# Kernel tuning notes

Measured on AMD Instinct MI355X. Metric: run time of the kernel, lower is better.

Reference implementation:

```python
import jax, jax.numpy as jnp
import numpy as np

N_ELEM = 10   # len(EnvPara.ELEMENTS)
N_ATOMS = 100000
N_DIM = 256


def setup_inputs() -> dict:
    key = jax.random.key(0)
    k = jax.random.split(key, 5)
    return {
        "input_tensor": jax.random.normal(k[0], (N_ATOMS, N_DIM), jnp.float32),
        "species": jax.random.randint(k[1], (N_ATOMS,), 0, N_ELEM, dtype=jnp.int64),
        "W1": jax.random.normal(k[2], (N_ELEM, N_DIM, N_DIM), jnp.float32) / np.sqrt(N_DIM).astype(np.float32),
        "b1": jnp.zeros((N_ELEM, N_DIM), jnp.float32),
        "W2": jax.random.normal(k[3], (N_ELEM, N_DIM, 1), jnp.float32) / np.sqrt(N_DIM).astype(np.float32),
        "b2": jnp.zeros((N_ELEM, 1), jnp.float32),
    }


def _element_linear(x, species, W, b):
    # Species-routed linear: each atom uses the weight/bias of its element.
    # Loop over the small fixed element set (N_ELEM=10) to avoid materializing
    # a [n_atoms, d_in, d_out] gathered-weight tensor.
    out = jnp.zeros((x.shape[0], W.shape[2]), dtype=x.dtype)
    for e in range(W.shape[0]):
        mask = (species == e)[:, None]                      # [n_atoms, 1]
        out = out + jnp.where(mask, x @ W[e] + b[e], jnp.zeros((), x.dtype))
    return out


def reference(input_tensor, species, W1, b1, W2, b2):
    # layer2(silu(layer1(x)))
    h = _element_linear(input_tensor, species, W1, b1)      # [n_atoms, n_dim]
    h = jax.nn.silu(h)                                      # way=0 -> plain SiLU
    return _element_linear(h, species, W2, b2)              # [n_atoms, 1]
```

## Files before the change

### kernel.cpp

```cpp
#include <hip/hip_runtime.h>
#include <hip/hip_bf16.h>
#include <stdint.h>


#define NDIM 256
#define CHUNKS 16
#define BCHUNK 16384
#define TROWS 32
#define ROWB 1040

typedef __attribute__((ext_vector_type(8))) short short8;
typedef __attribute__((ext_vector_type(8))) unsigned short ushort8;
typedef __attribute__((ext_vector_type(4))) float f32x4;

__device__ __forceinline__ unsigned short f2bf(float f) {
  unsigned u = __float_as_uint(f);
  u = (u + 0x7FFFu + ((u >> 16) & 1u)) >> 16;
  return (unsigned short)u;
}

__device__ __forceinline__ void gload_lds16(const void* gsrc, void* ldst) {
  __builtin_amdgcn_global_load_lds(
      (const __attribute__((address_space(1))) unsigned*)gsrc,
      (__attribute__((address_space(3))) unsigned*)(uintptr_t)(unsigned)(uintptr_t)ldst,
      16, 0, 0);
}

__device__ __forceinline__ short8 cvt8(float4 lo, float4 hi) {
  union { short8 s; unsigned u[4]; } r;
  __hip_bfloat162 t;
  t = __float22bfloat162_rn(make_float2(lo.x, lo.y)); r.u[0] = *(unsigned*)&t;
  t = __float22bfloat162_rn(make_float2(lo.z, lo.w)); r.u[1] = *(unsigned*)&t;
  t = __float22bfloat162_rn(make_float2(hi.x, hi.y)); r.u[2] = *(unsigned*)&t;
  t = __float22bfloat162_rn(make_float2(hi.z, hi.w)); r.u[3] = *(unsigned*)&t;
  return r.s;
}


__global__ void convw_k(const float* __restrict__ W1, unsigned short* __restrict__ wt, int NE) {
  int t = blockIdx.x * 256 + threadIdx.x;
  if (t >= NE * 8192) return;
  int n = t & 255;
  int g = (t >> 8) & 3;
  int step = (t >> 10) & 7;
  int e = t >> 13;
  int k0 = step * 32 + g * 8;
  const float* src = W1 + ((size_t)e << 16) + (size_t)k0 * NDIM + n;
  unsigned short v[8];
  #pragma unroll
  for (int j = 0; j < 8; ++j) v[j] = f2bf(src[j * NDIM]);
  char* chunk = (char*)wt + (size_t)(e * 8 + step) * BCHUNK;
  unsigned off = ((unsigned)(n * 64 + g * 16)) ^ ((unsigned)((n & 7) << 4));
  *(ushort8*)(chunk + off) = *(ushort8*)v;
}

__global__ void bhist_k(const int* __restrict__ sp, int n, int* __restrict__ bc, int NE) {
  __shared__ int wc[4][16];
  int tid = threadIdx.x;
  int i = blockIdx.x * 256 + tid;
  int s = (i < n) ? sp[i] : -1;
  int w = tid >> 6, lane = tid & 63;
  for (int e = 0; e < NE; ++e) {
    unsigned long long m = __ballot(s == e);
    if (lane == 0) wc[w][e] = __popcll(m);
  }
  __syncthreads();
  if (tid < NE) bc[blockIdx.x * NE + tid] = wc[0][tid] + wc[1][tid] + wc[2][tid] + wc[3][tid];
}

__global__ void scan_k(const int* __restrict__ bc, int* __restrict__ bo,
                       int* __restrict__ atom_start, int* __restrict__ tile_off,
                       int nblocks, int NE) {
  __shared__ int csum[256];
  __shared__ int coff[256];
  __shared__ int stot[16];
  __shared__ int sbase[16];
  int tid = threadIdx.x;
  int per = (nblocks + CHUNKS - 1) / CHUNKS;
  int e = tid / CHUNKS, c = tid % CHUNKS;
  int b0 = c * per, b1 = b0 + per; if (b1 > nblocks) b1 = nblocks;
  if (tid < NE * CHUNKS) {
    int s = 0;
    for (int b = b0; b < b1; ++b) s += bc[b * NE + e];
    csum[tid] = s;
  }
  __syncthreads();
  if (tid < NE) {
    int r = 0;
    for (int c2 = 0; c2 < CHUNKS; ++c2) { coff[tid * CHUNKS + c2] = r; r += csum[tid * CHUNKS + c2]; }
    stot[tid] = r;
  }
  __syncthreads();
  if (tid == 0) {
    int a = 0, t = 0;
    for (int e2 = 0; e2 < NE; ++e2) {
      sbase[e2] = a;
      atom_start[e2] = a; tile_off[e2] = t;
      a += stot[e2]; t += (stot[e2] + TROWS - 1) / TROWS;
    }
    atom_start[NE] = a; tile_off[NE] = t;
  }
  __syncthreads();
  if (tid < NE * CHUNKS) {
    int run = sbase[e] + coff[tid];
    for (int b = b0; b < b1; ++b) { bo[b * NE + e] = run; run += bc[b * NE + e]; }
  }
}

__global__ void dscatter_k(const int* __restrict__ sp, int n, const int* __restrict__ bo,
                           int* __restrict__ sorted, int NE) {
  __shared__ int wc[4][16];
  int tid = threadIdx.x;
  int i = blockIdx.x * 256 + tid;
  int s = (i < n) ? sp[i] : -1;
  int w = tid >> 6, lane = tid & 63;
  for (int e = 0; e < NE; ++e) {
    unsigned long long m = __ballot(s == e);
    if (lane == 0) wc[w][e] = __popcll(m);
  }
  __syncthreads();
  for (int e = 0; e < NE; ++e) {
    unsigned long long m = __ballot(s == e);
    if (s == e) {
      int wpre = 0;
      for (int w2 = 0; w2 < 4; ++w2) if (w2 < w) wpre += wc[w2][e];
      int rank = __popcll(m & ((1ull << lane) - 1ull));
      sorted[bo[blockIdx.x * NE + e] + wpre + rank] = i;
    }
  }
}


__global__ __launch_bounds__(512, 4) void gemm_k(
    const float* __restrict__ x, const unsigned short* __restrict__ wt,
    const float* __restrict__ b1, const float* __restrict__ w2,
    const float* __restrict__ b2, const int* __restrict__ sorted,
    const int* __restrict__ atom_start, const int* __restrict__ tile_off,
    float* __restrict__ out, int NE)
{
  __shared__ __align__(16) char smem[TROWS * ROWB + 1024];
  char* ldsA = smem;
  float* partLds = (float*)(smem + TROWS * ROWB);

  int b = blockIdx.x;
  if (b >= tile_off[NE]) return;
  int e = NE - 1;
  for (int i = 0; i < NE; ++i) { if (b < tile_off[i + 1]) { e = i; break; } }
  int t = b - tile_off[e];
  int rowStart = atom_start[e] + t * TROWS;
  int rowsValid = atom_start[e + 1] - rowStart;
  if (rowsValid > TROWS) rowsValid = TROWS;

  int tid = threadIdx.x;
  int lane = tid & 63, wid = tid >> 6;
  int lr = lane & 15, lg = lane >> 4;

  #pragma unroll
  for (int i = 0; i < 4; ++i) {
    int r = wid * 4 + i;
    int rr = (r < rowsValid) ? r : (rowsValid - 1);
    int atom = sorted[rowStart + rr];
    gload_lds16(x + (size_t)atom * NDIM + lane * 4, ldsA + r * ROWB);
  }

  const char* wbase = (const char*)wt + (size_t)e * 8 * BCHUNK;
  short8 bf[2][8];
  #pragma unroll
  for (int nf = 0; nf < 2; ++nf) {
    int n = wid * 32 + nf * 16 + lr;
    unsigned off = ((unsigned)(n * 64 + lg * 16)) ^ ((unsigned)((n & 7) << 4));
    #pragma unroll
    for (int s = 0; s < 8; ++s)
      bf[nf][s] = *(const short8*)(wbase + (size_t)s * BCHUNK + off);
  }

  f32x4 acc[2][2];
  const f32x4 zero = {0.f, 0.f, 0.f, 0.f};
  #pragma unroll
  for (int i = 0; i < 2; ++i)
    #pragma unroll
    for (int j = 0; j < 2; ++j) acc[i][j] = zero;

  __syncthreads();

  #pragma unroll
  for (int step = 0; step < 8; ++step) {
    int k0 = step * 32;
    short8 af[2];
    #pragma unroll
    for (int mf = 0; mf < 2; ++mf) {
      int r = mf * 16 + lr;
      const char* p = ldsA + r * ROWB + (k0 + lg * 8) * 4;
      float4 lo = *(const float4*)p;
      float4 hi = *(const float4*)(p + 16);
      af[mf] = cvt8(lo, hi);
    }
    #pragma unroll
    for (int mf = 0; mf < 2; ++mf)
      #pragma unroll
      for (int nf = 0; nf < 2; ++nf)
        acc[mf][nf] = __builtin_amdgcn_mfma_f32_16x16x32_bf16(af[mf], bf[nf][step], acc[mf][nf], 0, 0, 0);
  }

  const float* b1p = b1 + (size_t)e * NDIM;
  const float* w2p = w2 + (size_t)e * NDIM;
  float psum[2][4];
  #pragma unroll
  for (int mf = 0; mf < 2; ++mf)
    #pragma unroll
    for (int rg = 0; rg < 4; ++rg) psum[mf][rg] = 0.f;

  #pragma unroll
  for (int nf = 0; nf < 2; ++nf) {
    int ncol = wid * 32 + nf * 16 + lr;
    float bb = b1p[ncol];
    float wv = w2p[ncol];
    #pragma unroll
    for (int mf = 0; mf < 2; ++mf)
      #pragma unroll
      for (int rg = 0; rg < 4; ++rg) {
        float h = acc[mf][nf][rg] + bb;
        float sv = h * __builtin_amdgcn_rcpf(1.f + __expf(-h));
        psum[mf][rg] += sv * wv;
      }
  }

  #pragma unroll
  for (int mf = 0; mf < 2; ++mf)
    #pragma unroll
    for (int rg = 0; rg < 4; ++rg) {
      float v = psum[mf][rg];
      v += __shfl_xor(v, 1, 64);
      v += __shfl_xor(v, 2, 64);
      v += __shfl_xor(v, 4, 64);
      v += __shfl_xor(v, 8, 64);
      psum[mf][rg] = v;
    }

  if (lr == 0) {
    #pragma unroll
    for (int mf = 0; mf < 2; ++mf)
      #pragma unroll
      for (int rg = 0; rg < 4; ++rg)
        partLds[wid * TROWS + mf * 16 + lg * 4 + rg] = psum[mf][rg];
  }
  __syncthreads();
  if (tid < TROWS && tid < rowsValid) {
    float s = b2[e];
    #pragma unroll
    for (int w = 0; w < 8; ++w) s += partLds[w * TROWS + tid];
    out[sorted[rowStart + tid]] = s;
  }
}


extern "C" void kernel_launch(void* const* d_in, const int* in_sizes, int n_in,
                              void* d_out, int out_size, void* d_ws, size_t ws_size,
                              hipStream_t stream) {
  const float* x  = (const float*)d_in[0];
  const int*   sp = (const int*)d_in[1];
  const float* W1 = (const float*)d_in[2];
  const float* b1 = (const float*)d_in[3];
  const float* W2 = (const float*)d_in[4];
  const float* b2 = (const float*)d_in[5];
  float* out = (float*)d_out;

  int n_atoms = in_sizes[0] / NDIM;
  int NE = in_sizes[2] / (NDIM * NDIM);
  int nblocks = (n_atoms + 255) / 256;

  char* wsb = (char*)d_ws;
  size_t o = 0;
  int* bc = (int*)(wsb + o);         o += ((size_t)nblocks * NE * 4 + 255) & ~(size_t)255;
  int* bo = (int*)(wsb + o);         o += ((size_t)nblocks * NE * 4 + 255) & ~(size_t)255;
  int* atom_start = (int*)(wsb + o); o += 256;
  int* tile_off   = (int*)(wsb + o); o += 256;
  int* sorted     = (int*)(wsb + o); o += ((size_t)n_atoms * 4 + 255) & ~(size_t)255;
  unsigned short* wt = (unsigned short*)(wsb + o);

  hipLaunchKernelGGL(convw_k, dim3((NE * 8192 + 255) / 256), dim3(256), 0, stream,
                     W1, wt, NE);
  hipLaunchKernelGGL(bhist_k, dim3(nblocks), dim3(256), 0, stream, sp, n_atoms, bc, NE);
  hipLaunchKernelGGL(scan_k, dim3(1), dim3(256), 0, stream, bc, bo, atom_start, tile_off,
                     nblocks, NE);
  hipLaunchKernelGGL(dscatter_k, dim3(nblocks), dim3(256), 0, stream, sp, n_atoms, bo,
                     sorted, NE);

  int maxTiles = (n_atoms + TROWS - 1) / TROWS + NE;
  hipLaunchKernelGGL(gemm_k, dim3(maxTiles), dim3(512), 0, stream,
                     x, wt, b1, W2, b2, sorted, atom_start, tile_off, out, NE);
}
```

Before: 70.70 us.

## Make gemm kernel persistent with double-buffered row staging and weight reuse

The expert GEMM kernel becomes a persistent grid of 512 blocks, each walking a contiguous range of 32-row tiles. Per-element bf16 weight fragments, bias and W2 values stay in registers until the element changes, instead of being reloaded for every tile. The next tile's gathered input rows are prefetched into a second LDS buffer while the current tile is computed. The costs are doubled LDS per block, which may limit blocks per CU, and the risk of load imbalance from the static contiguous tile split.

New measurement: 69.83 us. Within noise of the previous version (-1.2%).

```diff
diff --git a/kernel.cpp b/kernel.cpp
--- a/kernel.cpp
+++ b/kernel.cpp
@@ -138,118 +138,140 @@
     const int* __restrict__ atom_start, const int* __restrict__ tile_off,
     float* __restrict__ out, int NE)
 {
-  __shared__ __align__(16) char smem[TROWS * ROWB + 1024];
-  char* ldsA = smem;
-  float* partLds = (float*)(smem + TROWS * ROWB);
-
-  int b = blockIdx.x;
-  if (b >= tile_off[NE]) return;
-  int e = NE - 1;
-  for (int i = 0; i < NE; ++i) { if (b < tile_off[i + 1]) { e = i; break; } }
-  int t = b - tile_off[e];
-  int rowStart = atom_start[e] + t * TROWS;
-  int rowsValid = atom_start[e + 1] - rowStart;
-  if (rowsValid > TROWS) rowsValid = TROWS;
-
-  int tid = threadIdx.x;
-  int lane = tid & 63, wid = tid >> 6;
+  __shared__ __align__(16) char ldsA[2][TROWS * ROWB];
+  __shared__ float partLds[256];
+  __shared__ int toffs[17], astart[17];
+
+  int tid = threadIdx.x, lane = tid & 63, wid = tid >> 6;
   int lr = lane & 15, lg = lane >> 4;
 
-  #pragma unroll
-  for (int i = 0; i < 4; ++i) {
-    int r = wid * 4 + i;
-    int rr = (r < rowsValid) ? r : (rowsValid - 1);
-    int atom = sorted[rowStart + rr];
-    gload_lds16(x + (size_t)atom * NDIM + lane * 4, ldsA + r * ROWB);
-  }
-
-  const char* wbase = (const char*)wt + (size_t)e * 8 * BCHUNK;
+  if (tid <= NE) { toffs[tid] = tile_off[tid]; astart[tid] = atom_start[tid]; }
+  __syncthreads();
+
+  int ntiles = toffs[NE];
+  int nb = gridDim.x, b = blockIdx.x;
+  int q = ntiles / nb, rem = ntiles % nb;
+  int t0 = b * q + (b < rem ? b : rem);
+  int cnt = q + (b < rem ? 1 : 0);
+  if (cnt <= 0) return;
+  int t1 = t0 + cnt;
+
+  int held_e = -1;
   short8 bf[2][8];
-  #pragma unroll
-  for (int nf = 0; nf < 2; ++nf) {
-    int n = wid * 32 + nf * 16 + lr;
-    unsigned off = ((unsigned)(n * 64 + lg * 16)) ^ ((unsigned)((n & 7) << 4));
-    #pragma unroll
-    for (int s = 0; s < 8; ++s)
-      bf[nf][s] = *(const short8*)(wbase + (size_t)s * BCHUNK + off);
-  }
-
-  f32x4 acc[2][2];
-  const f32x4 zero = {0.f, 0.f, 0.f, 0.f};
-  #pragma unroll
-  for (int i = 0; i < 2; ++i)
-    #pragma unroll
-    for (int j = 0; j < 2; ++j) acc[i][j] = zero;
-
-  __syncthreads();
-
-  #pragma unroll
-  for (int step = 0; step < 8; ++step) {
-    int k0 = step * 32;
-    short8 af[2];
-    #pragma unroll
-    for (int mf = 0; mf < 2; ++mf) {
-      int r = mf * 16 + lr;
-      const char* p = ldsA + r * ROWB + (k0 + lg * 8) * 4;
-      float4 lo = *(const float4*)p;
-      float4 hi = *(const float4*)(p + 16);
-      af[mf] = cvt8(lo, hi);
-    }
+  float bbv[2], wvv[2], b2v = 0.f;
+
+  auto stageA = [&](int t, int buf) {
+    int e = 0;
+    while (t >= toffs[e + 1]) ++e;
+    int rs = astart[e] + (t - toffs[e]) * TROWS;
+    int rv = astart[e + 1] - rs; if (rv > TROWS) rv = TROWS;
+    #pragma unroll
+    for (int i = 0; i < 4; ++i) {
+      int rrow = wid * 4 + i;
+      int rcl = (rrow < rv) ? rrow : (rv - 1);
+      int atom = sorted[rs + rcl];
+      gload_lds16(x + (size_t)atom * NDIM + lane * 4, &ldsA[buf][rrow * ROWB]);
+    }
+  };
+
+  stageA(t0, 0);
+
+  for (int t = t0; t < t1; ++t) {
+    int buf = (t - t0) & 1;
+    int e = 0;
+    while (t >= toffs[e + 1]) ++e;
+    int rs = astart[e] + (t - toffs[e]) * TROWS;
+    int rv = astart[e + 1] - rs; if (rv > TROWS) rv = TROWS;
+
+    if (e != held_e) {
+      held_e = e;
+      const char* wbase = (const char*)wt + (size_t)e * 8 * BCHUNK;
+      #pragma unroll
+      for (int nf = 0; nf < 2; ++nf) {
+        int ncol = wid * 32 + nf * 16 + lr;
+        unsigned off = ((unsigned)(ncol * 64 + lg * 16)) ^ ((unsigned)((ncol & 7) << 4));
+        #pragma unroll
+        for (int s = 0; s < 8; ++s)
+          bf[nf][s] = *(const short8*)(wbase + (size_t)s * BCHUNK + off);
+        bbv[nf] = b1[(size_t)e * NDIM + ncol];
+        wvv[nf] = w2[(size_t)e * NDIM + ncol];
+      }
+      b2v = b2[e];
+    }
+
+    __syncthreads();
+    if (t + 1 < t1) stageA(t + 1, buf ^ 1);
+
+    f32x4 acc[2][2];
+    const f32x4 zero = {0.f, 0.f, 0.f, 0.f};
+    #pragma unroll
+    for (int i = 0; i < 2; ++i)
+      #pragma unroll
+      for (int j = 0; j < 2; ++j) acc[i][j] = zero;
+
+    const char* Ab = ldsA[buf];
+    #pragma unroll
+    for (int step = 0; step < 8; ++step) {
+      int k0 = step * 32;
+      short8 af[2];
+      #pragma unroll
+      for (int mf = 0; mf < 2; ++mf) {
+        const char* p = Ab + (mf * 16 + lr) * ROWB + (k0 + lg * 8) * 4;
+        float4 lo = *(const float4*)p;
+        float4 hi = *(const float4*)(p + 16);
+        af[mf] = cvt8(lo, hi);
+      }
+      #pragma unroll
+      for (int mf = 0; mf < 2; ++mf)
+        #pragma unroll
+        for (int nf = 0; nf < 2; ++nf)
+          acc[mf][nf] = __builtin_amdgcn_mfma_f32_16x16x32_bf16(af[mf], bf[nf][step], acc[mf][nf], 0, 0, 0);
+    }
+
+    float psum[2][4];
     #pragma unroll
     for (int mf = 0; mf < 2; ++mf)
       #pragma unroll
-      for (int nf = 0; nf < 2; ++nf)
-        acc[mf][nf] = __builtin_amdgcn_mfma_f32_16x16x32_bf16(af[mf], bf[nf][step], acc[mf][nf], 0, 0, 0);
-  }
-
-  const float* b1p = b1 + (size_t)e * NDIM;
-  const float* w2p = w2 + (size_t)e * NDIM;
-  float psum[2][4];
-  #pragma unroll
-  for (int mf = 0; mf < 2; ++mf)
-    #pragma unroll
-    for (int rg = 0; rg < 4; ++rg) psum[mf][rg] = 0.f;
-
-  #pragma unroll
-  for (int nf = 0; nf < 2; ++nf) {
-    int ncol = wid * 32 + nf * 16 + lr;
-    float bb = b1p[ncol];
-    float wv = w2p[ncol];
+      for (int rg = 0; rg < 4; ++rg) psum[mf][rg] = 0.f;
+
+    #pragma unroll
+    for (int nf = 0; nf < 2; ++nf) {
+      #pragma unroll
+      for (int mf = 0; mf < 2; ++mf)
+        #pragma unroll
+        for (int rg = 0; rg < 4; ++rg) {
+          float h = acc[mf][nf][rg] + bbv[nf];
+          float sv = h * __builtin_amdgcn_rcpf(1.f + __expf(-h));
+          psum[mf][rg] += sv * wvv[nf];
+        }
+    }
     #pragma unroll
     for (int mf = 0; mf < 2; ++mf)
       #pragma unroll
       for (int rg = 0; rg < 4; ++rg) {
-        float h = acc[mf][nf][rg] + bb;
-        float sv = h * __builtin_amdgcn_rcpf(1.f + __expf(-h));
-        psum[mf][rg] += sv * wv;
+        float v = psum[mf][rg];
+        v += __shfl_xor(v, 1, 64);
+        v += __shfl_xor(v, 2, 64);
+        v += __shfl_xor(v, 4, 64);
+        v += __shfl_xor(v, 8, 64);
+        psum[mf][rg] = v;
       }
-  }
-
-  #pragma unroll
-  for (int mf = 0; mf < 2; ++mf)
-    #pragma unroll
-    for (int rg = 0; rg < 4; ++rg) {
-      float v = psum[mf][rg];
-      v += __shfl_xor(v, 1, 64);
-      v += __shfl_xor(v, 2, 64);
-      v += __shfl_xor(v, 4, 64);
-      v += __shfl_xor(v, 8, 64);
-      psum[mf][rg] = v;
-    }
-
-  if (lr == 0) {
-    #pragma unroll
-    for (int mf = 0; mf < 2; ++mf)
-      #pragma unroll
-      for (int rg = 0; rg < 4; ++rg)
-        partLds[wid * TROWS + mf * 16 + lg * 4 + rg] = psum[mf][rg];
-  }
-  __syncthreads();
-  if (tid < TROWS && tid < rowsValid) {
-    float s = b2[e];
-    #pragma unroll
-    for (int w = 0; w < 8; ++w) s += partLds[w * TROWS + tid];
-    out[sorted[rowStart + tid]] = s;
+    if (lr == 0) {
+      #pragma unroll
+      for (int mf = 0; mf < 2; ++mf)
+        #pragma unroll
+        for (int rg = 0; rg < 4; ++rg)
+          partLds[wid * TROWS + mf * 16 + lg * 4 + rg] = psum[mf][rg];
+    }
+
+    asm volatile("s_waitcnt lgkmcnt(0)\n\ts_barrier" ::: "memory");
+
+    if (tid < TROWS && tid < rv) {
+      float s = b2v;
+      #pragma unroll
+      for (int w = 0; w < 8; ++w) s += partLds[w * TROWS + tid];
+      out[sorted[rs + tid]] = s;
+    }
   }
 }
 
@@ -286,7 +308,6 @@
   hipLaunchKernelGGL(dscatter_k, dim3(nblocks), dim3(256), 0, stream, sp, n_atoms, bo,
                      sorted, NE);
 
-  int maxTiles = (n_atoms + TROWS - 1) / TROWS + NE;
-  hipLaunchKernelGGL(gemm_k, dim3(maxTiles), dim3(512), 0, stream,
+  hipLaunchKernelGGL(gemm_k, dim3(512), dim3(512), 0, stream,
                      x, wt, b1, W2, b2, sorted, atom_start, tile_off, out, NE);
 }
```
